# Performance work log

Measured on AMD Instinct MI355X. Metric: run time of the kernel, lower is better.

## Reference

```python
import jax, jax.numpy as jnp
import numpy as np

N = 100000          # nodes
F_IN = 500          # num_features
HID = 256           # hidden
C = 40              # out_classes
E = 2302585         # ~ N*ln(N)*ec, doubled (both directions) in spar_samp
ALPHA0 = 0.1        # att[0][0] = alpha*(1-alpha)**0


def setup_inputs() -> dict:
    key = jax.random.key(0)
    ks = jax.random.split(key, 8)
    x = jax.random.normal(ks[0], (N, F_IN), dtype=jnp.float32)
    W1 = jax.random.normal(ks[1], (F_IN, HID), dtype=jnp.float32) * (1.0 / np.sqrt(F_IN))
    b1 = jnp.zeros((HID,), dtype=jnp.float32)
    W2 = jax.random.normal(ks[2], (HID, C), dtype=jnp.float32) * (1.0 / np.sqrt(HID))
    b2 = jnp.zeros((C,), dtype=jnp.float32)
    edge_row = jax.random.randint(ks[3], (E,), 0, N, dtype=jnp.int64) if jax.config.jax_enable_x64 else jax.random.randint(ks[3], (E,), 0, N, dtype=jnp.int32)
    edge_col = jax.random.randint(ks[4], (E,), 0, N, dtype=edge_row.dtype)
    # sampled importance weights: deg^{-1/2}*deg^{-1/2}*(M/num_edgess) -> small positive floats
    edge_val = jax.random.uniform(ks[5], (E,), dtype=jnp.float32, minval=0.001, maxval=0.05)
    return {"x": x, "W1": W1, "b1": b1, "W2": W2, "b2": b2,
            "edge_row": edge_row, "edge_col": edge_col, "edge_val": edge_val}


def reference(x, W1, b1, W2, b2, edge_row, edge_col, edge_val):
    # eval mode: dropout is identity
    h = jax.nn.relu(x @ W1 + b1)          # [N, HID]
    h = h @ W2 + b2                       # [N, C]
    # sparse propagation: out[r] += val * h[c]  (scatter-add SpMM)
    msg = edge_val[:, None] * h[edge_col]            # [E, C] gather
    agg = jax.ops.segment_sum(msg, edge_row, num_segments=N)  # [N, C]
    out = h * ALPHA0 + agg
    return jax.nn.log_softmax(out, axis=1)
```

## Files before the change

### kernel.cpp

```cpp
#include <hip/hip_runtime.h>
#include <hip/hip_bf16.h>


#define N_NODES 100000
#define F_IN    500
#define HID     256
#define C_OUT   40
#define ALPHA0  0.1f
#define H2STRIDE 64

#define RPB     64
#define NBUCK   ((N_NODES + RPB - 1) / RPB)
#define NBUCKP  1568
#define NCH     256
#define SCAN_M  (NBUCK * NCH)
#define SCAN_CHUNK 2048
#define NBS     ((SCAN_M + SCAN_CHUNK - 1) / SCAN_CHUNK)
#define BCAPL   1792

typedef short short8 __attribute__((ext_vector_type(8)));
typedef float f32x4  __attribute__((ext_vector_type(4)));

__device__ __forceinline__ short f2bf(float f) {
  union { float f; unsigned u; } x; x.f = f;
  unsigned r = x.u + 0x7fffu + ((x.u >> 16) & 1u);
  return (short)(r >> 16);
}
__device__ __forceinline__ float bf2f(short s) {
  union { unsigned u; float f; } x; x.u = ((unsigned)(unsigned short)s) << 16;
  return x.f;
}
__device__ __forceinline__ unsigned cvtpk(float lo, float hi) {
  unsigned r;
  asm("v_cvt_pk_bf16_f32 %0, %1, %2" : "=v"(r) : "v"(lo), "v"(hi));
  return r;
}
__device__ __forceinline__ void lbar() {
  asm volatile("s_waitcnt lgkmcnt(0)" ::: "memory");
  __builtin_amdgcn_s_barrier();
}
__device__ __forceinline__ void gll16(const float* g, const char* l) {
  __builtin_amdgcn_global_load_lds(
      (const __attribute__((address_space(1))) void*)g,
      (__attribute__((address_space(3))) void*)l, 16, 0, 0);
}

__global__ __launch_bounds__(256) void k_pack_weights(
    const float* __restrict__ W1, const float* __restrict__ W2,
    short* __restrict__ W1S, short* __restrict__ W2T)
{
  int i = blockIdx.x * 256 + threadIdx.x;
  if (i < 16*256*32) {
    int kc  = i >> 13;
    int idx = i & 8191;
    int n   = idx >> 5;
    int kk  = idx & 31;
    int k   = kc*32 + kk;
    float v = (k < F_IN) ? W1[k*HID + n] : 0.f;
    W1S[i] = f2bf(v);
  } else {
    int j = i - 16*256*32;
    if (j < 48*256) {
      int n = j >> 8;
      int k = j & 255;
      float v = (n < C_OUT) ? W2[k*C_OUT + n] : 0.f;
      W2T[j] = f2bf(v);
    }
  }
}

__global__ __launch_bounds__(512, 4) void k_fused_mlp(
    const float* __restrict__ x, const float* __restrict__ b1v,
    const float* __restrict__ b2v,
    const short* __restrict__ W1S, const short* __restrict__ W2T,
    short* __restrict__ h2b,
    const int* __restrict__ erow, int* __restrict__ hs, int E, int CH)
{
  __shared__ __align__(16) char smem[65536];
  short (*Hl)[256] = (short(*)[256])smem;

  const int tid  = threadIdx.x;
  const int w    = tid >> 6;
  const int lane = tid & 63;
  const int lr   = lane & 15;
  const int quad = lane >> 4;
  const int wr   = w >> 2;
  const int wc   = w & 3;
  const int row0 = blockIdx.x * 128;

  const int s_rl0 = (w*2)*8 + (lane>>3);
  const int s_rl1 = (w*2+1)*8 + (lane>>3);
  const int ksw   = ((lane&7) ^ ((lane>>3)&7)) * 4;
  const float* gp0 = x + (size_t)min(row0 + s_rl0, N_NODES-1) * F_IN;
  const float* gp1 = x + (size_t)min(row0 + s_rl1, N_NODES-1) * F_IN;
  const char* l0 = smem + (w*2)*1024;
  const char* l1 = smem + (w*2+1)*1024;

  f32x4 acc[4][4] = {};

  #pragma unroll
  for (int p = 0; p < 2; ++p) {
    int kb = p*32 + ksw;
    const float* a0 = (kb + 4 <= F_IN) ? gp0 + kb : x;
    const float* a1 = (kb + 4 <= F_IN) ? gp1 + kb : x;
    gll16(a0, l0 + p*16384);
    gll16(a1, l1 + p*16384);
  }

  const short* bbase = W1S + (wc*64 + lr)*32 + quad*8;
  const int m2 = lr & 7;

  #pragma unroll
  for (int kc = 0; kc < 16; ++kc) {
    short8 bf4[4];
    #pragma unroll
    for (int t = 0; t < 4; ++t)
      bf4[t] = *(const short8*)(bbase + kc*8192 + t*16*32);
    __builtin_amdgcn_sched_barrier(0);

    if (kc < 14) {
      int kb = (kc+2)*32 + ksw;
      const float* a0 = (kb + 4 <= F_IN) ? gp0 + kb : x;
      const float* a1 = (kb + 4 <= F_IN) ? gp1 + kb : x;
      gll16(a0, l0 + ((kc+2)&3)*16384);
      gll16(a1, l1 + ((kc+2)&3)*16384);
      __builtin_amdgcn_sched_barrier(0);
      asm volatile("s_waitcnt vmcnt(8)" ::: "memory");
    } else if (kc == 14) {
      asm volatile("s_waitcnt vmcnt(6)" ::: "memory");
    } else {
      asm volatile("s_waitcnt vmcnt(4)" ::: "memory");
    }
    __builtin_amdgcn_s_barrier();

    const char* Abase = smem + (kc & 3)*16384;
    short8 af[4];
    #pragma unroll
    for (int t = 0; t < 4; ++t) {
      int rl = wr*64 + t*16 + lr;
      f32x4 u0 = *(const f32x4*)(Abase + rl*128 + (((quad*2  ) ^ m2) << 4));
      f32x4 u1 = *(const f32x4*)(Abase + rl*128 + (((quad*2+1) ^ m2) << 4));
      union { unsigned u[4]; short8 s; } pk;
      pk.u[0] = cvtpk(u0[0], u0[1]);
      pk.u[1] = cvtpk(u0[2], u0[3]);
      pk.u[2] = cvtpk(u1[0], u1[1]);
      pk.u[3] = cvtpk(u1[2], u1[3]);
      af[t] = pk.s;
    }

    #pragma unroll
    for (int rt = 0; rt < 4; ++rt)
      #pragma unroll
      for (int ct = 0; ct < 4; ++ct)
        acc[rt][ct] = __builtin_amdgcn_mfma_f32_16x16x32_bf16(af[rt], bf4[ct], acc[rt][ct], 0, 0, 0);
  }
  lbar();

  #pragma unroll
  for (int ct = 0; ct < 4; ++ct) {
    int col = wc*64 + ct*16 + lr;
    int cg = col >> 3, ci = col & 7;
    float bias = b1v[col];
    #pragma unroll
    for (int rt = 0; rt < 4; ++rt) {
      #pragma unroll
      for (int r = 0; r < 4; ++r) {
        int row = wr*64 + rt*16 + quad*4 + r;
        float v = fmaxf(acc[rt][ct][r] + bias, 0.f);
        Hl[row][((cg ^ (row & 31)) << 3) | ci] = f2bf(v);
      }
    }
  }
  lbar();

  f32x4 acc2[3] = {};
  const int arow = w*16 + lr;
  #pragma unroll
  for (int kc2 = 0; kc2 < 8; ++kc2) {
    int gg = kc2*4 + quad;
    short8 a2 = *(const short8*)&Hl[arow][(gg ^ (arow & 31)) << 3];
    #pragma unroll
    for (int nt = 0; nt < 3; ++nt) {
      short8 b2 = *(const short8*)(W2T + (nt*16 + lr)*256 + kc2*32 + quad*8);
      acc2[nt] = __builtin_amdgcn_mfma_f32_16x16x32_bf16(a2, b2, acc2[nt], 0, 0, 0);
    }
  }

  #pragma unroll
  for (int nt = 0; nt < 3; ++nt) {
    int col = nt*16 + lr;
    float bias = (col < C_OUT) ? b2v[col] : 0.f;
    #pragma unroll
    for (int r = 0; r < 4; ++r) {
      int row = row0 + w*16 + quad*4 + r;
      if (row < N_NODES) {
        float v = (col < C_OUT) ? (acc2[nt][r] + bias) : 0.f;
        h2b[(long)row * H2STRIDE + col] = f2bf(v);
      }
    }
  }
  {
    int col = 48 + lr;
    #pragma unroll
    for (int r = 0; r < 4; ++r) {
      int row = row0 + w*16 + quad*4 + r;
      if (row < N_NODES) h2b[(long)row * H2STRIDE + col] = 0;
    }
  }

  if (blockIdx.x < NCH) {
    int cc = blockIdx.x;
    int* hcnt = (int*)smem;
    lbar();
    for (int b = tid; b < NBUCK; b += 512) hcnt[b] = 0;
    __syncthreads();
    int e0 = cc * CH, e1 = min(E, e0 + CH);
    if (e0 < e1) {
      int g0 = e0 >> 2, g1 = e1 >> 2;
      const int4* rp = (const int4*)erow;
      for (int g = g0 + tid; g < g1; g += 512) {
        int4 r4 = rp[g];
        atomicAdd(&hcnt[r4.x >> 6], 1);
        atomicAdd(&hcnt[r4.y >> 6], 1);
        atomicAdd(&hcnt[r4.z >> 6], 1);
        atomicAdd(&hcnt[r4.w >> 6], 1);
      }
      for (int e = (g1 << 2) + tid; e < e1; e += 512)
        atomicAdd(&hcnt[erow[e] >> 6], 1);
    }
    __syncthreads();
    for (int b = tid; b < NBUCK; b += 512)
      hs[(size_t)cc * NBUCKP + b] = hcnt[b];
  }
}

__global__ __launch_bounds__(256) void k_transpose(
    const int* __restrict__ hs, int* __restrict__ offs)
{
  __shared__ int t[64][65];
  int cb = blockIdx.x & 3;
  int bb = blockIdx.x >> 2;
  int c0 = cb * 64, b0 = bb * 64;
  int j  = threadIdx.x & 63;
  int i0 = threadIdx.x >> 6;
  #pragma unroll
  for (int k = 0; k < 16; ++k) {
    int i = i0 + k * 4;
    int b = b0 + j;
    t[i][j] = (b < NBUCK) ? hs[(size_t)(c0 + i) * NBUCKP + b] : 0;
  }
  __syncthreads();
  #pragma unroll
  for (int k = 0; k < 16; ++k) {
    int i = i0 + k * 4;
    int b = b0 + i;
    if (b < NBUCK) offs[(size_t)b * NCH + c0 + j] = t[j][i];
  }
}

__global__ __launch_bounds__(256) void k_scan1(
    int* __restrict__ offs, int* __restrict__ bsums)
{
  __shared__ int sh[256];
  int tid = threadIdx.x;
  int base = blockIdx.x * SCAN_CHUNK + tid * 8;
  int d[8];
  #pragma unroll
  for (int k = 0; k < 8; ++k)
    d[k] = (base + k < SCAN_M) ? offs[base + k] : 0;
  int s = 0;
  #pragma unroll
  for (int k = 0; k < 8; ++k) s += d[k];
  sh[tid] = s;
  __syncthreads();
  for (int o = 1; o < 256; o <<= 1) {
    int v = (tid >= o) ? sh[tid - o] : 0;
    __syncthreads();
    if (tid >= o) sh[tid] += v;
    __syncthreads();
  }
  int run = sh[tid] - s;
  #pragma unroll
  for (int k = 0; k < 8; ++k) {
    if (base + k < SCAN_M) offs[base + k] = run;
    run += d[k];
  }
  if (tid == 255) bsums[blockIdx.x] = sh[255];
}

__global__ __launch_bounds__(256) void k_scan2(int* __restrict__ bsums) {
  __shared__ int sh[256];
  int tid = threadIdx.x;
  int v = (tid < NBS) ? bsums[tid] : 0;
  sh[tid] = v;
  __syncthreads();
  for (int o = 1; o < 256; o <<= 1) {
    int u = (tid >= o) ? sh[tid - o] : 0;
    __syncthreads();
    if (tid >= o) sh[tid] += u;
    __syncthreads();
  }
  if (tid < NBS) bsums[tid] = sh[tid] - v;
}

__global__ __launch_bounds__(512) void k_split(
    const int* __restrict__ erow, const int* __restrict__ ecol,
    const float* __restrict__ eval, const int* __restrict__ offs,
    const int* __restrict__ bsums, int2* __restrict__ sorted,
    int* __restrict__ bstart, int E, int CH)
{
  __shared__ int cur[NBUCK];
  int tid = threadIdx.x, c = blockIdx.x;

  for (int b = tid; b < NBUCK; b += 512) {
    int m = b * NCH + c;
    int val = offs[m] + bsums[m >> 11];
    cur[b] = val;
    if (c == 0) bstart[b] = val;
  }
  if (c == 0 && tid == 0) bstart[NBUCK] = E;
  __syncthreads();

  int e0 = c * CH, e1 = min(E, e0 + CH);
  if (e0 >= e1) return;
  int g0 = e0 >> 2, g1 = e1 >> 2;
  const int4*   rp = (const int4*)erow;
  const int4*   cp = (const int4*)ecol;
  const float4* vp = (const float4*)eval;
  for (int g = g0 + tid; g < g1; g += 512) {
    int4 r4 = rp[g];
    int4 c4 = cp[g];
    float4 v4 = vp[g];
    int p0 = atomicAdd(&cur[r4.x >> 6], 1);
    int p1 = atomicAdd(&cur[r4.y >> 6], 1);
    int p2 = atomicAdd(&cur[r4.z >> 6], 1);
    int p3 = atomicAdd(&cur[r4.w >> 6], 1);
    int2 cv;
    cv.x = c4.x | ((r4.x & 63) << 17); cv.y = __float_as_int(v4.x); sorted[p0] = cv;
    cv.x = c4.y | ((r4.y & 63) << 17); cv.y = __float_as_int(v4.y); sorted[p1] = cv;
    cv.x = c4.z | ((r4.z & 63) << 17); cv.y = __float_as_int(v4.z); sorted[p2] = cv;
    cv.x = c4.w | ((r4.w & 63) << 17); cv.y = __float_as_int(v4.w); sorted[p3] = cv;
  }
  for (int e = (g1 << 2) + tid; e < e1; e += 512) {
    int r = erow[e];
    int pos = atomicAdd(&cur[r >> 6], 1);
    int2 cv;
    cv.x = ecol[e] | ((r & 63) << 17);
    cv.y = __float_as_int(eval[e]);
    sorted[pos] = cv;
  }
}

__global__ __launch_bounds__(256) void k_csr_spmm(
    const int* __restrict__ bstart, const int2* __restrict__ sorted,
    const short* __restrict__ h2b, float* __restrict__ out)
{
  __shared__ int2 eS[BCAPL];
  __shared__ int h[RPB];
  __shared__ int roff[RPB];
  __shared__ int cur[RPB];
  int tid = threadIdx.x, b = blockIdx.x;
  int lane = tid & 63, w = tid >> 6;
  int start = bstart[b], end = bstart[b + 1];
  int cnt = end - start;

  if (tid < RPB) h[tid] = 0;
  __syncthreads();
  for (int i = tid; i < cnt; i += 256)
    atomicAdd(&h[((unsigned)sorted[start + i].x) >> 17], 1);
  __syncthreads();
  if (w == 0) {
    int v = h[lane];
    int hv = v;
    #pragma unroll
    for (int o = 1; o < 64; o <<= 1) {
      int t = __shfl_up(v, o);
      if (lane >= o) v += t;
    }
    roff[lane] = v;
    cur[lane]  = v - hv;
  }
  __syncthreads();
  for (int i = tid; i < cnt; i += 256) {
    int2 cv = sorted[start + i];
    int p = atomicAdd(&cur[((unsigned)cv.x) >> 17], 1);
    if (p < BCAPL) eS[p] = cv;
  }
  __syncthreads();

  for (int rr = 0; rr < 16; ++rr) {
    int r = w * 16 + rr;
    int row = b * RPB + r;
    if (row >= N_NODES) continue;
    float acc = ALPHA0 * bf2f(h2b[(size_t)row * H2STRIDE + lane]);
    int e  = roff[r] - h[r];
    int ee = roff[r];
    for (; e + 7 < ee; e += 8) {
      int2 cc[8];
      float gg[8];
      #pragma unroll
      for (int j = 0; j < 8; ++j) cc[j] = eS[e + j];
      #pragma unroll
      for (int j = 0; j < 8; ++j)
        gg[j] = bf2f(h2b[(size_t)(cc[j].x & 0x1FFFF) * H2STRIDE + lane]);
      #pragma unroll
      for (int j = 0; j < 8; ++j) acc += __int_as_float(cc[j].y) * gg[j];
    }
    for (; e + 3 < ee; e += 4) {
      int2 c0 = eS[e], c1 = eS[e+1], c2 = eS[e+2], c3 = eS[e+3];
      float g0 = bf2f(h2b[(size_t)(c0.x & 0x1FFFF) * H2STRIDE + lane]);
      float g1 = bf2f(h2b[(size_t)(c1.x & 0x1FFFF) * H2STRIDE + lane]);
      float g2 = bf2f(h2b[(size_t)(c2.x & 0x1FFFF) * H2STRIDE + lane]);
      float g3 = bf2f(h2b[(size_t)(c3.x & 0x1FFFF) * H2STRIDE + lane]);
      acc += __int_as_float(c0.y) * g0;
      acc += __int_as_float(c1.y) * g1;
      acc += __int_as_float(c2.y) * g2;
      acc += __int_as_float(c3.y) * g3;
    }
    for (; e < ee; ++e) {
      int2 c0 = eS[e];
      acc += __int_as_float(c0.y) * bf2f(h2b[(size_t)(c0.x & 0x1FFFF) * H2STRIDE + lane]);
    }
    float m = (lane < C_OUT) ? acc : -INFINITY;
    #pragma unroll
    for (int o = 32; o > 0; o >>= 1) m = fmaxf(m, __shfl_xor(m, o));
    float ev = (lane < C_OUT) ? __expf(acc - m) : 0.f;
    float s = ev;
    #pragma unroll
    for (int o = 32; o > 0; o >>= 1) s += __shfl_xor(s, o);
    if (lane < C_OUT) out[(long)row * C_OUT + lane] = acc - m - __logf(s);
  }
}

extern "C" void kernel_launch(void* const* d_in, const int* in_sizes, int n_in,
                              void* d_out, int out_size, void* d_ws, size_t ws_size,
                              hipStream_t stream) {
  const float* x    = (const float*)d_in[0];
  const float* W1   = (const float*)d_in[1];
  const float* b1   = (const float*)d_in[2];
  const float* W2   = (const float*)d_in[3];
  const float* b2   = (const float*)d_in[4];
  const int*   erow = (const int*)d_in[5];
  const int*   ecol = (const int*)d_in[6];
  const float* eval = (const float*)d_in[7];
  const int E  = in_sizes[5];
  int CH = (E + NCH - 1) / NCH;
  CH = (CH + 3) & ~3;

  char* p = (char*)d_ws;
  short* h2b    = (short*)p;  p += (size_t)N_NODES * H2STRIDE * 2;
  short* W1S    = (short*)p;  p += (size_t)16*256*32 * 2;
  short* W2T    = (short*)p;  p += (size_t)48*256 * 2;
  int*   hs     = (int*)p;    p += (size_t)NCH * NBUCKP * 4;
  int*   offs   = (int*)p;    p += (size_t)SCAN_M * 4;
  int*   bsums  = (int*)p;    p += 256 * 4;
  int*   bstart = (int*)p;    p += (size_t)(NBUCK + 4) * 4;
  int2*  sorted = (int2*)p;
  float* out = (float*)d_out;

  k_pack_weights<<<(16*256*32 + 48*256 + 255)/256, 256, 0, stream>>>(W1, W2, W1S, W2T);
  k_fused_mlp<<<(N_NODES + 127)/128, 512, 0, stream>>>(x, b1, b2, W1S, W2T, h2b,
                                                       erow, hs, E, CH);
  k_transpose<<<4 * 25, 256, 0, stream>>>(hs, offs);
  k_scan1<<<NBS, 256, 0, stream>>>(offs, bsums);
  k_scan2<<<1, 256, 0, stream>>>(bsums);
  k_split<<<NCH, 512, 0, stream>>>(erow, ecol, eval, offs, bsums, sorted, bstart, E, CH);
  k_csr_spmm<<<NBUCK, 256, 0, stream>>>(bstart, sorted, h2b, out);
}
```

Measured before the change: 478.8 us.

## Replace global bucket scan with per-chunk local offsets and gather segments in SpMM

Each edge chunk now computes an exclusive scan of its own bucket histogram inside the MLP kernel, and k_split writes edges into a chunk-private region of the sorted buffer. This removes the global two-level scan kernels and their launches. The SpMM kernel (now 512 threads) reads the transposed per-chunk offsets, scans the 256 segment counts, and gathers each bucket's edges from 256 scattered segments into shared memory. The cost is many short, uncoalesced segment reads per bucket in exchange for fewer kernels and less global scan traffic.

```diff
diff --git a/kernel.cpp b/kernel.cpp
--- a/kernel.cpp
+++ b/kernel.cpp
@@ -13,9 +13,6 @@
 #define NBUCK   ((N_NODES + RPB - 1) / RPB)
 #define NBUCKP  1568
 #define NCH     256
-#define SCAN_M  (NBUCK * NCH)
-#define SCAN_CHUNK 2048
-#define NBS     ((SCAN_M + SCAN_CHUNK - 1) / SCAN_CHUNK)
 #define BCAPL   1792
 
 typedef short short8 __attribute__((ext_vector_type(8)));
@@ -74,7 +71,7 @@
     const float* __restrict__ b2v,
     const short* __restrict__ W1S, const short* __restrict__ W2T,
     short* __restrict__ h2b,
-    const int* __restrict__ erow, int* __restrict__ hs, int E, int CH)
+    const int* __restrict__ erow, int* __restrict__ lofs, int E, int CH)
 {
   __shared__ __align__(16) char smem[65536];
   short (*Hl)[256] = (short(*)[256])smem;
@@ -211,8 +208,9 @@
   if (blockIdx.x < NCH) {
     int cc = blockIdx.x;
     int* hcnt = (int*)smem;
+    int* ssum = (int*)(smem + NBUCKP * 4);
     lbar();
-    for (int b = tid; b < NBUCK; b += 512) hcnt[b] = 0;
+    for (int b = tid; b < NBUCKP; b += 512) hcnt[b] = 0;
     __syncthreads();
     int e0 = cc * CH, e1 = min(E, e0 + CH);
     if (e0 < e1) {
@@ -229,13 +227,34 @@
         atomicAdd(&hcnt[erow[e] >> 6], 1);
     }
     __syncthreads();
-    for (int b = tid; b < NBUCK; b += 512)
-      hs[(size_t)cc * NBUCKP + b] = hcnt[b];
+    int base = tid * 4;
+    int d0 = 0, d1 = 0, d2 = 0, d3 = 0, s = 0;
+    if (base < NBUCKP) {
+      d0 = hcnt[base]; d1 = hcnt[base+1]; d2 = hcnt[base+2]; d3 = hcnt[base+3];
+      s = d0 + d1 + d2 + d3;
+    }
+    ssum[tid] = s;
+    __syncthreads();
+    for (int o = 1; o < 512; o <<= 1) {
+      int u = (tid >= o) ? ssum[tid - o] : 0;
+      __syncthreads();
+      if (tid >= o) ssum[tid] += u;
+      __syncthreads();
+    }
+    if (base < NBUCKP) {
+      int run = ssum[tid] - s;
+      int4 wv;
+      wv.x = run;
+      wv.y = run + d0;
+      wv.z = run + d0 + d1;
+      wv.w = run + d0 + d1 + d2;
+      *(int4*)&lofs[(size_t)cc * NBUCKP + base] = wv;
+    }
   }
 }
 
 __global__ __launch_bounds__(256) void k_transpose(
-    const int* __restrict__ hs, int* __restrict__ offs)
+    const int* __restrict__ lofs, int* __restrict__ lofsT)
 {
   __shared__ int t[64][65];
   int cb = blockIdx.x & 3;
@@ -247,80 +266,30 @@
   for (int k = 0; k < 16; ++k) {
     int i = i0 + k * 4;
     int b = b0 + j;
-    t[i][j] = (b < NBUCK) ? hs[(size_t)(c0 + i) * NBUCKP + b] : 0;
+    t[i][j] = (b <= NBUCK) ? lofs[(size_t)(c0 + i) * NBUCKP + b] : 0;
   }
   __syncthreads();
   #pragma unroll
   for (int k = 0; k < 16; ++k) {
     int i = i0 + k * 4;
     int b = b0 + i;
-    if (b < NBUCK) offs[(size_t)b * NCH + c0 + j] = t[j][i];
-  }
-}
-
-__global__ __launch_bounds__(256) void k_scan1(
-    int* __restrict__ offs, int* __restrict__ bsums)
-{
-  __shared__ int sh[256];
-  int tid = threadIdx.x;
-  int base = blockIdx.x * SCAN_CHUNK + tid * 8;
-  int d[8];
-  #pragma unroll
-  for (int k = 0; k < 8; ++k)
-    d[k] = (base + k < SCAN_M) ? offs[base + k] : 0;
-  int s = 0;
-  #pragma unroll
-  for (int k = 0; k < 8; ++k) s += d[k];
-  sh[tid] = s;
-  __syncthreads();
-  for (int o = 1; o < 256; o <<= 1) {
-    int v = (tid >= o) ? sh[tid - o] : 0;
-    __syncthreads();
-    if (tid >= o) sh[tid] += v;
-    __syncthreads();
-  }
-  int run = sh[tid] - s;
-  #pragma unroll
-  for (int k = 0; k < 8; ++k) {
-    if (base + k < SCAN_M) offs[base + k] = run;
-    run += d[k];
-  }
-  if (tid == 255) bsums[blockIdx.x] = sh[255];
-}
-
-__global__ __launch_bounds__(256) void k_scan2(int* __restrict__ bsums) {
-  __shared__ int sh[256];
-  int tid = threadIdx.x;
-  int v = (tid < NBS) ? bsums[tid] : 0;
-  sh[tid] = v;
-  __syncthreads();
-  for (int o = 1; o < 256; o <<= 1) {
-    int u = (tid >= o) ? sh[tid - o] : 0;
-    __syncthreads();
-    if (tid >= o) sh[tid] += u;
-    __syncthreads();
-  }
-  if (tid < NBS) bsums[tid] = sh[tid] - v;
+    if (b <= NBUCK) lofsT[(size_t)b * NCH + c0 + j] = t[j][i];
+  }
 }
 
 __global__ __launch_bounds__(512) void k_split(
     const int* __restrict__ erow, const int* __restrict__ ecol,
-    const float* __restrict__ eval, const int* __restrict__ offs,
-    const int* __restrict__ bsums, int2* __restrict__ sorted,
-    int* __restrict__ bstart, int E, int CH)
+    const float* __restrict__ eval, const int* __restrict__ lofs,
+    int2* __restrict__ sorted, int E, int CH)
 {
   __shared__ int cur[NBUCK];
   int tid = threadIdx.x, c = blockIdx.x;
 
-  for (int b = tid; b < NBUCK; b += 512) {
-    int m = b * NCH + c;
-    int val = offs[m] + bsums[m >> 11];
-    cur[b] = val;
-    if (c == 0) bstart[b] = val;
-  }
-  if (c == 0 && tid == 0) bstart[NBUCK] = E;
-  __syncthreads();
-
+  for (int b = tid; b < NBUCK; b += 512)
+    cur[b] = lofs[(size_t)c * NBUCKP + b];
+  __syncthreads();
+
+  size_t obase = (size_t)c * CH;
   int e0 = c * CH, e1 = min(E, e0 + CH);
   if (e0 >= e1) return;
   int g0 = e0 >> 2, g1 = e1 >> 2;
@@ -336,10 +305,10 @@
     int p2 = atomicAdd(&cur[r4.z >> 6], 1);
     int p3 = atomicAdd(&cur[r4.w >> 6], 1);
     int2 cv;
-    cv.x = c4.x | ((r4.x & 63) << 17); cv.y = __float_as_int(v4.x); sorted[p0] = cv;
-    cv.x = c4.y | ((r4.y & 63) << 17); cv.y = __float_as_int(v4.y); sorted[p1] = cv;
-    cv.x = c4.z | ((r4.z & 63) << 17); cv.y = __float_as_int(v4.z); sorted[p2] = cv;
-    cv.x = c4.w | ((r4.w & 63) << 17); cv.y = __float_as_int(v4.w); sorted[p3] = cv;
+    cv.x = c4.x | ((r4.x & 63) << 17); cv.y = __float_as_int(v4.x); sorted[obase + p0] = cv;
+    cv.x = c4.y | ((r4.y & 63) << 17); cv.y = __float_as_int(v4.y); sorted[obase + p1] = cv;
+    cv.x = c4.z | ((r4.z & 63) << 17); cv.y = __float_as_int(v4.z); sorted[obase + p2] = cv;
+    cv.x = c4.w | ((r4.w & 63) << 17); cv.y = __float_as_int(v4.w); sorted[obase + p3] = cv;
   }
   for (int e = (g1 << 2) + tid; e < e1; e += 512) {
     int r = erow[e];
@@ -347,27 +316,55 @@
     int2 cv;
     cv.x = ecol[e] | ((r & 63) << 17);
     cv.y = __float_as_int(eval[e]);
-    sorted[pos] = cv;
-  }
-}
-
-__global__ __launch_bounds__(256) void k_csr_spmm(
-    const int* __restrict__ bstart, const int2* __restrict__ sorted,
-    const short* __restrict__ h2b, float* __restrict__ out)
+    sorted[obase + pos] = cv;
+  }
+}
+
+__global__ __launch_bounds__(512) void k_csr_spmm(
+    const int* __restrict__ lofsT, const int2* __restrict__ sorted,
+    const short* __restrict__ h2b, float* __restrict__ out, int CH)
 {
+  __shared__ int2 eraw[BCAPL];
   __shared__ int2 eS[BCAPL];
-  __shared__ int h[RPB];
-  __shared__ int roff[RPB];
-  __shared__ int cur[RPB];
+  __shared__ int sA[NCH];
+  __shared__ int cntc[NCH];
+  __shared__ int cpos[NCH];
+  __shared__ int h[RPB], roff[RPB], cur[RPB];
   int tid = threadIdx.x, b = blockIdx.x;
   int lane = tid & 63, w = tid >> 6;
-  int start = bstart[b], end = bstart[b + 1];
-  int cnt = end - start;
-
+
+  if (tid < NCH) {
+    int a  = lofsT[(size_t)b * NCH + tid];
+    int e2 = lofsT[(size_t)(b + 1) * NCH + tid];
+    sA[tid]   = a;
+    cntc[tid] = e2 - a;
+    cpos[tid] = e2 - a;
+  }
   if (tid < RPB) h[tid] = 0;
   __syncthreads();
-  for (int i = tid; i < cnt; i += 256)
-    atomicAdd(&h[((unsigned)sorted[start + i].x) >> 17], 1);
+  for (int o = 1; o < NCH; o <<= 1) {
+    int u = (tid >= o && tid < NCH) ? cpos[tid - o] : 0;
+    __syncthreads();
+    if (tid >= o && tid < NCH) cpos[tid] += u;
+    __syncthreads();
+  }
+  int cntT = min(cpos[NCH - 1], BCAPL);
+
+  {
+    int c    = tid & (NCH - 1);
+    int half = tid >> 8;
+    int srcb = c * CH + sA[c];
+    int dstb = cpos[c] - cntc[c];
+    int n    = cntc[c];
+    for (int k = half; k < n; k += 2) {
+      int p = dstb + k;
+      if (p < BCAPL) {
+        int2 cv = sorted[srcb + k];
+        eraw[p] = cv;
+        atomicAdd(&h[((unsigned)cv.x) >> 17], 1);
+      }
+    }
+  }
   __syncthreads();
   if (w == 0) {
     int v = h[lane];
@@ -381,15 +378,15 @@
     cur[lane]  = v - hv;
   }
   __syncthreads();
-  for (int i = tid; i < cnt; i += 256) {
-    int2 cv = sorted[start + i];
+  for (int i = tid; i < cntT; i += 512) {
+    int2 cv = eraw[i];
     int p = atomicAdd(&cur[((unsigned)cv.x) >> 17], 1);
     if (p < BCAPL) eS[p] = cv;
   }
   __syncthreads();
 
-  for (int rr = 0; rr < 16; ++rr) {
-    int r = w * 16 + rr;
+  for (int rr = 0; rr < 8; ++rr) {
+    int r = w * 8 + rr;
     int row = b * RPB + r;
     if (row >= N_NODES) continue;
     float acc = ALPHA0 * bf2f(h2b[(size_t)row * H2STRIDE + lane]);
@@ -451,19 +448,15 @@
   short* h2b    = (short*)p;  p += (size_t)N_NODES * H2STRIDE * 2;
   short* W1S    = (short*)p;  p += (size_t)16*256*32 * 2;
   short* W2T    = (short*)p;  p += (size_t)48*256 * 2;
-  int*   hs     = (int*)p;    p += (size_t)NCH * NBUCKP * 4;
-  int*   offs   = (int*)p;    p += (size_t)SCAN_M * 4;
-  int*   bsums  = (int*)p;    p += 256 * 4;
-  int*   bstart = (int*)p;    p += (size_t)(NBUCK + 4) * 4;
+  int*   lofs   = (int*)p;    p += (size_t)NCH * NBUCKP * 4;
+  int*   lofsT  = (int*)p;    p += (size_t)1600 * NCH * 4;
   int2*  sorted = (int2*)p;
   float* out = (float*)d_out;
 
   k_pack_weights<<<(16*256*32 + 48*256 + 255)/256, 256, 0, stream>>>(W1, W2, W1S, W2T);
   k_fused_mlp<<<(N_NODES + 127)/128, 512, 0, stream>>>(x, b1, b2, W1S, W2T, h2b,
-                                                       erow, hs, E, CH);
-  k_transpose<<<4 * 25, 256, 0, stream>>>(hs, offs);
-  k_scan1<<<NBS, 256, 0, stream>>>(offs, bsums);
-  k_scan2<<<1, 256, 0, stream>>>(bsums);
-  k_split<<<NCH, 512, 0, stream>>>(erow, ecol, eval, offs, bsums, sorted, bstart, E, CH);
-  k_csr_spmm<<<NBUCK, 256, 0, stream>>>(bstart, sorted, h2b, out);
-}
+                                                       erow, lofs, E, CH);
+  k_transpose<<<4 * 25, 256, 0, stream>>>(lofs, lofsT);
+  k_split<<<NCH, 512, 0, stream>>>(erow, ecol, eval, lofs, sorted, E, CH);
+  k_csr_spmm<<<NBUCK, 512, 0, stream>>>(lofsT, sorted, h2b, out, CH);
+}
```

Measured after the change: 463.2 us. 3.3% less time.
